# Performance work log

Measured on AMD Instinct MI355X. Metric: run time of the kernel, lower is better.

## Reference

```python
import jax, jax.numpy as jnp
import numpy as np


def _affine_grid(params, B, H, W):
    # torch F.affine_grid semantics, align_corners=False
    tx = params[:, 0] / W
    ty = params[:, 1] / H
    theta = params[:, 2]
    c = jnp.cos(theta)[:, None, None]   # (B,1,1)
    s = jnp.sin(theta)[:, None, None]
    # base normalized coords (pixel-center convention for align_corners=False)
    xs = (2.0 * jnp.arange(W, dtype=params.dtype) + 1.0) / W - 1.0  # (W,)
    ys = (2.0 * jnp.arange(H, dtype=params.dtype) + 1.0) / H - 1.0  # (H,)
    xs = xs[None, None, :]   # (1,1,W)
    ys = ys[None, :, None]   # (1,H,1)
    gx = c * xs - s * ys + tx[:, None, None]  # (B,H,W)
    gy = s * xs + c * ys + ty[:, None, None]  # (B,H,W)
    return gx, gy


def _bilinear_sample_one(im, gx, gy):
    # im: (C,H,W); gx,gy: (H,W) normalized coords in [-1,1]
    # grid_sample align_corners=False, padding_mode='zeros'
    C, H, W = im.shape
    ix = ((gx + 1.0) * W - 1.0) * 0.5
    iy = ((gy + 1.0) * H - 1.0) * 0.5
    x0f = jnp.floor(ix)
    y0f = jnp.floor(iy)
    x0 = x0f.astype(jnp.int32)
    y0 = y0f.astype(jnp.int32)
    x1 = x0 + 1
    y1 = y0 + 1
    wx1 = ix - x0f
    wx0 = 1.0 - wx1
    wy1 = iy - y0f
    wy0 = 1.0 - wy1

    def gather(yc, xc):
        valid = ((xc >= 0) & (xc < W) & (yc >= 0) & (yc < H)).astype(im.dtype)
        xcc = jnp.clip(xc, 0, W - 1)
        ycc = jnp.clip(yc, 0, H - 1)
        return im[:, ycc, xcc] * valid[None]  # (C,H,W)

    out = (gather(y0, x0) * (wy0 * wx0)[None]
           + gather(y0, x1) * (wy0 * wx1)[None]
           + gather(y1, x0) * (wy1 * wx0)[None]
           + gather(y1, x1) * (wy1 * wx1)[None])
    return out


def setup_inputs() -> dict:
    key = jax.random.key(0)
    k1, k2 = jax.random.split(key)
    img = jax.random.normal(k1, (16, 8, 512, 512), dtype=jnp.float32)
    params = jax.random.normal(k2, (16, 3), dtype=jnp.float32)
    return {"img": img, "params": params}


def reference(img, params):
    B, C, H, W = img.shape
    gx, gy = _affine_grid(params, B, H, W)  # (B,H,W) each
    return jax.vmap(_bilinear_sample_one)(img, gx, gy)  # (B,C,H,W)
```

## Files before the change

kernel.cpp:

```cpp
#include <hip/hip_runtime.h>
#include <math.h>

constexpr int B = 16, C = 8, H = 512, W = 512;
constexpr int HW = H * W;
constexpr int TILE = 32;
constexpr int LDS_FLOATS = 2400;

__global__ __launch_bounds__(256) void grid_sampler_kernel(
    const float* __restrict__ img,
    const float* __restrict__ params,
    float* __restrict__ out) {
    __shared__ float lds[LDS_FLOATS];
    const int tid = threadIdx.x;
    const int blk = blockIdx.x;
    const int b   = blk >> 8;
    const int tt  = blk & 255;
    const int ty0 = (tt >> 4) * TILE;
    const int tx0 = (tt & 15) * TILE;

    const float tpx = params[b * 3 + 0] * (1.0f / W);
    const float tpy = params[b * 3 + 1] * (1.0f / H);
    const float th  = params[b * 3 + 2];
    const float c = cosf(th), s = sinf(th);

    auto srcxy = [&](float x, float y, float& ix, float& iy) {
        float xs = (2.0f * x + 1.0f) * (1.0f / W) - 1.0f;
        float ys = (2.0f * y + 1.0f) * (1.0f / H) - 1.0f;
        float gx = c * xs - s * ys + tpx;
        float gy = s * xs + c * ys + tpy;
        ix = ((gx + 1.0f) * (float)W - 1.0f) * 0.5f;
        iy = ((gy + 1.0f) * (float)H - 1.0f) * 0.5f;
    };

    float ixa, iya, ixb, iyb, ixc, iyc, ixd, iyd;
    srcxy((float)tx0,            (float)ty0,            ixa, iya);
    srcxy((float)(tx0 + TILE-1), (float)ty0,            ixb, iyb);
    srcxy((float)tx0,            (float)(ty0 + TILE-1), ixc, iyc);
    srcxy((float)(tx0 + TILE-1), (float)(ty0 + TILE-1), ixd, iyd);
    const float ixmin = fminf(fminf(ixa, ixb), fminf(ixc, ixd));
    const float ixmax = fmaxf(fmaxf(ixa, ixb), fmaxf(ixc, ixd));
    const float iymin = fminf(fminf(iya, iyb), fminf(iyc, iyd));
    const float iymax = fmaxf(fmaxf(iya, iyb), fmaxf(iyc, iyd));
    const int xlo = min(max((int)floorf(ixmin), 0), W - 1);
    const int xhi = min(max((int)floorf(ixmax) + 1, 0), W - 1);
    const int ylo = min(max((int)floorf(iymin), 0), H - 1);
    const int yhi = min(max((int)floorf(iymax) + 1, 0), H - 1);
    const int bw = xhi - xlo + 1;
    const int bh = yhi - ylo + 1;
    const int stride = bw | 1;

    const int ox  = tx0 + (tid & 31);
    const int oyb = ty0 + (tid >> 5);
    int   o00[4], o01[4], o10[4], o11[4], ooff[4];
    float w00[4], w01[4], w10[4], w11[4];
#pragma unroll
    for (int k = 0; k < 4; ++k) {
        const int oy = oyb + 8 * k;
        float ix, iy;
        srcxy((float)ox, (float)oy, ix, iy);
        const float x0f = floorf(ix), y0f = floorf(iy);
        const int x0 = (int)x0f, y0 = (int)y0f;
        const int x1 = x0 + 1,  y1 = y0 + 1;
        const float wx1 = ix - x0f, wx0 = 1.0f - wx1;
        const float wy1 = iy - y0f, wy0 = 1.0f - wy1;
        const float vx0 = (x0 >= 0 && x0 < W) ? 1.0f : 0.0f;
        const float vx1 = (x1 >= 0 && x1 < W) ? 1.0f : 0.0f;
        const float vy0 = (y0 >= 0 && y0 < H) ? 1.0f : 0.0f;
        const float vy1 = (y1 >= 0 && y1 < H) ? 1.0f : 0.0f;
        w00[k] = wy0 * wx0 * vy0 * vx0;
        w01[k] = wy0 * wx1 * vy0 * vx1;
        w10[k] = wy1 * wx0 * vy1 * vx0;
        w11[k] = wy1 * wx1 * vy1 * vx1;
        const int x0c = min(max(x0, 0), W - 1) - xlo;
        const int x1c = min(max(x1, 0), W - 1) - xlo;
        const int y0c = min(max(y0, 0), H - 1) - ylo;
        const int y1c = min(max(y1, 0), H - 1) - ylo;
        o00[k] = y0c * stride + x0c;
        o01[k] = y0c * stride + x1c;
        o10[k] = y1c * stride + x0c;
        o11[k] = y1c * stride + x1c;
        ooff[k] = oy * W + ox;
    }

    const size_t batoff = (size_t)b * C * HW;
    const float* iplane = img + batoff + (size_t)ylo * W + xlo;
    float*       oplane = out + batoff;
    const int lx = tid & 63, ry = tid >> 6;

    for (int ch = 0; ch < C; ++ch) {
        if (lx < bw) {
            for (int r = ry; r < bh; r += 4)
                lds[r * stride + lx] = iplane[(size_t)ch * HW + r * W + lx];
        }
        __syncthreads();
#pragma unroll
        for (int k = 0; k < 4; ++k) {
            float v = lds[o00[k]] * w00[k] + lds[o01[k]] * w01[k]
                    + lds[o10[k]] * w10[k] + lds[o11[k]] * w11[k];
            oplane[(size_t)ch * HW + ooff[k]] = v;
        }
        __syncthreads();
    }
}

extern "C" void kernel_launch(void* const* d_in, const int* in_sizes, int n_in,
                              void* d_out, int out_size, void* d_ws, size_t ws_size,
                              hipStream_t stream) {
    const float* img    = (const float*)d_in[0];
    const float* params = (const float*)d_in[1];
    float*       out    = (float*)d_out;

    constexpr int grid = B * (H / TILE) * (W / TILE);
    grid_sampler_kernel<<<grid, 256, 0, stream>>>(img, params, out);
}
```

Measured before the change: 266.1 us.

## Interleave channel pairs in LDS as float2 and halve barrier count

Stages two channels at once into LDS as interleaved float2 values, with a one-column halo and a padded stride. Each output pixel then does four 8-byte LDS reads that serve two channels, and the kernel runs four iterations with barriers instead of eight. Index computation is simplified to two base offsets per pixel. LDS use grows to 20KB, which may reduce occupancy, and the halo and clamping logic must stay correct at image edges.

```diff
diff --git a/kernel.cpp b/kernel.cpp
--- a/kernel.cpp
+++ b/kernel.cpp
@@ -4,13 +4,13 @@
 constexpr int B = 16, C = 8, H = 512, W = 512;
 constexpr int HW = H * W;
 constexpr int TILE = 32;
-constexpr int LDS_FLOATS = 2400;
+constexpr int MAXPOS = 2560;
 
 __global__ __launch_bounds__(256) void grid_sampler_kernel(
     const float* __restrict__ img,
     const float* __restrict__ params,
     float* __restrict__ out) {
-    __shared__ float lds[LDS_FLOATS];
+    __shared__ float2 lds2[MAXPOS];
     const int tid = threadIdx.x;
     const int blk = blockIdx.x;
     const int b   = blk >> 8;
@@ -47,11 +47,12 @@
     const int yhi = min(max((int)floorf(iymax) + 1, 0), H - 1);
     const int bw = xhi - xlo + 1;
     const int bh = yhi - ylo + 1;
-    const int stride = bw | 1;
+    const int xlo_s = xlo - 1;
+    const int stride = (bw + 2) | 1;
 
     const int ox  = tx0 + (tid & 31);
     const int oyb = ty0 + (tid >> 5);
-    int   o00[4], o01[4], o10[4], o11[4], ooff[4];
+    int   base0[4], base1[4], ooff[4];
     float w00[4], w01[4], w10[4], w11[4];
 #pragma unroll
     for (int k = 0; k < 4; ++k) {
@@ -71,33 +72,38 @@
         w01[k] = wy0 * wx1 * vy0 * vx1;
         w10[k] = wy1 * wx0 * vy1 * vx0;
         w11[k] = wy1 * wx1 * vy1 * vx1;
-        const int x0c = min(max(x0, 0), W - 1) - xlo;
-        const int x1c = min(max(x1, 0), W - 1) - xlo;
-        const int y0c = min(max(y0, 0), H - 1) - ylo;
-        const int y1c = min(max(y1, 0), H - 1) - ylo;
-        o00[k] = y0c * stride + x0c;
-        o01[k] = y0c * stride + x1c;
-        o10[k] = y1c * stride + x0c;
-        o11[k] = y1c * stride + x1c;
-        ooff[k] = oy * W + ox;
+        const int xi  = min(max(x0 - xlo_s, 0), stride - 1);
+        const int yi0 = min(max(y0 - ylo, 0), bh - 1);
+        const int yi1 = min(max(y1 - ylo, 0), bh - 1);
+        base0[k] = yi0 * stride + xi;
+        base1[k] = yi1 * stride + xi;
+        ooff[k]  = oy * W + ox;
     }
 
     const size_t batoff = (size_t)b * C * HW;
-    const float* iplane = img + batoff + (size_t)ylo * W + xlo;
-    float*       oplane = out + batoff;
     const int lx = tid & 63, ry = tid >> 6;
 
-    for (int ch = 0; ch < C; ++ch) {
-        if (lx < bw) {
+    for (int g = 0; g < 4; ++g) {
+        const float* p0 = img + batoff + (size_t)(2 * g) * HW + (size_t)ylo * W;
+        const float* p1 = p0 + HW;
+        if (lx <= stride) {
+            const int col = min(max(xlo_s + lx, 0), W - 1);
             for (int r = ry; r < bh; r += 4)
-                lds[r * stride + lx] = iplane[(size_t)ch * HW + r * W + lx];
+                lds2[r * stride + lx] = make_float2(p0[r * W + col], p1[r * W + col]);
         }
         __syncthreads();
+        float* o0 = out + batoff + (size_t)(2 * g) * HW;
+        float* o1 = o0 + HW;
 #pragma unroll
         for (int k = 0; k < 4; ++k) {
-            float v = lds[o00[k]] * w00[k] + lds[o01[k]] * w01[k]
-                    + lds[o10[k]] * w10[k] + lds[o11[k]] * w11[k];
-            oplane[(size_t)ch * HW + ooff[k]] = v;
+            const float2 t00 = lds2[base0[k]], t01 = lds2[base0[k] + 1];
+            const float2 t10 = lds2[base1[k]], t11 = lds2[base1[k] + 1];
+            const float vx = t00.x * w00[k] + t01.x * w01[k]
+                           + t10.x * w10[k] + t11.x * w11[k];
+            const float vy = t00.y * w00[k] + t01.y * w01[k]
+                           + t10.y * w10[k] + t11.y * w11[k];
+            o0[ooff[k]] = vx;
+            o1[ooff[k]] = vy;
         }
         __syncthreads();
     }
```

New measurement: 260.5 us. -2.1%, faster.

## Double-buffer LDS tiles via global_load_lds DMA and vectorize output stores

Applied to the files above, without the earlier changes.

Replaces the per-channel synchronous global-to-LDS copy with direct global_load_lds DMA into a double-buffered fixed 48x64 source window, prefetching the next channel while the current one is sampled. Thread mapping changes so each thread computes four adjacent output pixels and writes them as one float4 store. It assumes the rotated source footprint always fits in a 48-row by 64-column window (clamping indices otherwise), which may be wrong for large rotations where the footprint exceeds that size.

```diff
diff --git a/kernel.cpp b/kernel.cpp
--- a/kernel.cpp
+++ b/kernel.cpp
@@ -4,19 +4,33 @@
 constexpr int B = 16, C = 8, H = 512, W = 512;
 constexpr int HW = H * W;
 constexpr int TILE = 32;
-constexpr int LDS_FLOATS = 2400;
+constexpr int ROWS = 48;
+constexpr int LSTR = 79;
+constexpr int BUFSZ = ROWS * LSTR;
+
+__device__ __forceinline__ void dma4(const float* g, float* l) {
+    __builtin_amdgcn_global_load_lds(
+        (const __attribute__((address_space(1))) unsigned int*)g,
+        (__attribute__((address_space(3))) unsigned int*)l,
+        4, 0, 0);
+}
 
 __global__ __launch_bounds__(256) void grid_sampler_kernel(
     const float* __restrict__ img,
     const float* __restrict__ params,
     float* __restrict__ out) {
-    __shared__ float lds[LDS_FLOATS];
+    __shared__ float lds[2][BUFSZ];
     const int tid = threadIdx.x;
     const int blk = blockIdx.x;
     const int b   = blk >> 8;
     const int tt  = blk & 255;
     const int ty0 = (tt >> 4) * TILE;
     const int tx0 = (tt & 15) * TILE;
+
+    if (tid < 96) {
+        const int bb = tid / ROWS, r = tid % ROWS;
+        lds[bb][r * LSTR + 64] = 0.0f;
+    }
 
     const float tpx = params[b * 3 + 0] * (1.0f / W);
     const float tpy = params[b * 3 + 1] * (1.0f / H);
@@ -33,31 +47,25 @@
     };
 
     float ixa, iya, ixb, iyb, ixc, iyc, ixd, iyd;
-    srcxy((float)tx0,            (float)ty0,            ixa, iya);
-    srcxy((float)(tx0 + TILE-1), (float)ty0,            ixb, iyb);
-    srcxy((float)tx0,            (float)(ty0 + TILE-1), ixc, iyc);
-    srcxy((float)(tx0 + TILE-1), (float)(ty0 + TILE-1), ixd, iyd);
+    srcxy((float)tx0,             (float)ty0,             ixa, iya);
+    srcxy((float)(tx0 + TILE-1),  (float)ty0,             ixb, iyb);
+    srcxy((float)tx0,             (float)(ty0 + TILE-1),  ixc, iyc);
+    srcxy((float)(tx0 + TILE-1),  (float)(ty0 + TILE-1),  ixd, iyd);
     const float ixmin = fminf(fminf(ixa, ixb), fminf(ixc, ixd));
-    const float ixmax = fmaxf(fmaxf(ixa, ixb), fmaxf(ixc, ixd));
     const float iymin = fminf(fminf(iya, iyb), fminf(iyc, iyd));
-    const float iymax = fmaxf(fmaxf(iya, iyb), fmaxf(iyc, iyd));
     const int xlo = min(max((int)floorf(ixmin), 0), W - 1);
-    const int xhi = min(max((int)floorf(ixmax) + 1, 0), W - 1);
     const int ylo = min(max((int)floorf(iymin), 0), H - 1);
-    const int yhi = min(max((int)floorf(iymax) + 1, 0), H - 1);
-    const int bw = xhi - xlo + 1;
-    const int bh = yhi - ylo + 1;
-    const int stride = bw | 1;
+    const int xls = xlo - 1;
+    const int yls = min(ylo, H - ROWS);
 
-    const int ox  = tx0 + (tid & 31);
-    const int oyb = ty0 + (tid >> 5);
-    int   o00[4], o01[4], o10[4], o11[4], ooff[4];
+    const int oy  = ty0 + (tid >> 3);
+    const int oxb = tx0 + (tid & 7) * 4;
+    int   a0[4], a1[4];
     float w00[4], w01[4], w10[4], w11[4];
 #pragma unroll
-    for (int k = 0; k < 4; ++k) {
-        const int oy = oyb + 8 * k;
+    for (int j = 0; j < 4; ++j) {
         float ix, iy;
-        srcxy((float)ox, (float)oy, ix, iy);
+        srcxy((float)(oxb + j), (float)oy, ix, iy);
         const float x0f = floorf(ix), y0f = floorf(iy);
         const int x0 = (int)x0f, y0 = (int)y0f;
         const int x1 = x0 + 1,  y1 = y0 + 1;
@@ -67,39 +75,57 @@
         const float vx1 = (x1 >= 0 && x1 < W) ? 1.0f : 0.0f;
         const float vy0 = (y0 >= 0 && y0 < H) ? 1.0f : 0.0f;
         const float vy1 = (y1 >= 0 && y1 < H) ? 1.0f : 0.0f;
-        w00[k] = wy0 * wx0 * vy0 * vx0;
-        w01[k] = wy0 * wx1 * vy0 * vx1;
-        w10[k] = wy1 * wx0 * vy1 * vx0;
-        w11[k] = wy1 * wx1 * vy1 * vx1;
-        const int x0c = min(max(x0, 0), W - 1) - xlo;
-        const int x1c = min(max(x1, 0), W - 1) - xlo;
-        const int y0c = min(max(y0, 0), H - 1) - ylo;
-        const int y1c = min(max(y1, 0), H - 1) - ylo;
-        o00[k] = y0c * stride + x0c;
-        o01[k] = y0c * stride + x1c;
-        o10[k] = y1c * stride + x0c;
-        o11[k] = y1c * stride + x1c;
-        ooff[k] = oy * W + ox;
+        w00[j] = wy0 * wx0 * vy0 * vx0;
+        w01[j] = wy0 * wx1 * vy0 * vx1;
+        w10[j] = wy1 * wx0 * vy1 * vx0;
+        w11[j] = wy1 * wx1 * vy1 * vx1;
+        const int xi  = min(max(x0 - xls, 0), 63);
+        const int yi0 = min(max(y0 - yls, 0), ROWS - 1);
+        const int yi1 = min(max(y1 - yls, 0), ROWS - 1);
+        a0[j] = yi0 * LSTR + xi;
+        a1[j] = yi1 * LSTR + xi;
     }
 
     const size_t batoff = (size_t)b * C * HW;
-    const float* iplane = img + batoff + (size_t)ylo * W + xlo;
-    float*       oplane = out + batoff;
-    const int lx = tid & 63, ry = tid >> 6;
+    const int ooff = oy * W + oxb;
+    const int wv = tid >> 6, ln = tid & 63;
+    const int scol = min(max(xls + ln, 0), W - 1);
+    const float* sbase = img + batoff + (size_t)yls * W + scol;
 
-    for (int ch = 0; ch < C; ++ch) {
-        if (lx < bw) {
-            for (int r = ry; r < bh; r += 4)
-                lds[r * stride + lx] = iplane[(size_t)ch * HW + r * W + lx];
+#pragma unroll
+    for (int j2 = 0; j2 < 12; ++j2) {
+        const int r = 12 * wv + j2;
+        dma4(sbase + (size_t)r * W, &lds[0][r * LSTR]);
+    }
+
+#pragma unroll
+    for (int g = 0; g < 8; ++g) {
+        if (g < 7) {
+            const float* sp = sbase + (size_t)(g + 1) * HW;
+            float* dp = &lds[(g + 1) & 1][0];
+#pragma unroll
+            for (int j2 = 0; j2 < 12; ++j2) {
+                const int r = 12 * wv + j2;
+                dma4(sp + (size_t)r * W, dp + r * LSTR);
+            }
+            asm volatile("s_waitcnt vmcnt(12) lgkmcnt(0)\n\ts_barrier" ::: "memory");
+        } else {
+            asm volatile("s_waitcnt vmcnt(0) lgkmcnt(0)\n\ts_barrier" ::: "memory");
         }
-        __syncthreads();
+
+        const float* bp = &lds[g & 1][0];
+        float4 v;
 #pragma unroll
-        for (int k = 0; k < 4; ++k) {
-            float v = lds[o00[k]] * w00[k] + lds[o01[k]] * w01[k]
-                    + lds[o10[k]] * w10[k] + lds[o11[k]] * w11[k];
-            oplane[(size_t)ch * HW + ooff[k]] = v;
+        for (int j = 0; j < 4; ++j) {
+            const float t00 = bp[a0[j]], t01 = bp[a0[j] + 1];
+            const float t10 = bp[a1[j]], t11 = bp[a1[j] + 1];
+            ((float*)&v)[j] = t00 * w00[j] + t01 * w01[j]
+                            + t10 * w10[j] + t11 * w11[j];
         }
-        __syncthreads();
+        *(float4*)(out + batoff + (size_t)g * HW + ooff) = v;
+
+        if (g < 7)
+            asm volatile("s_waitcnt lgkmcnt(0)\n\ts_barrier" ::: "memory");
     }
 }
 
```

Result: faster. 242.5 us (-8.8%).
